# Kernel tuning notes

Measured on AMD Instinct MI355X. Metric: run time of the kernel, lower is better.

The kernel has to match this reference:

```python
import jax, jax.numpy as jnp
import numpy as np

# Vim-S config
B, L, D, DEPTH = 16, 197, 384, 24
DI, DS, DTR = 768, 16, 24  # d_inner=2*D, d_state, dt_rank=ceil(D/16)
NUM_CLASSES = 1000
EPS = 1e-5


def setup_inputs() -> dict:
    key = jax.random.key(0)
    ks = jax.random.split(key, 12)
    f = jnp.float32
    rn = lambda k, shp, s=0.02: jax.random.normal(k, shp, f) * s
    inp = {
        'x': jax.random.normal(ks[0], (B, 3, 224, 224), f),
        'patch_w': rn(ks[1], (D, 3, 16, 16)),
        'patch_b': jnp.zeros((D,), f),
        'cls_token': rn(ks[2], (1, 1, D)),
        'pos_embed': rn(ks[3], (1, L, D)),
        'in_proj_w': rn(ks[4], (DEPTH, 2 * DI, D)),
        'conv_w': rn(ks[5], (DEPTH, DI, 1, 4), 0.1),  # depthwise causal conv, d_conv=4
        'conv_b': jnp.zeros((DEPTH, DI), f),
        'x_proj_w': rn(ks[6], (DEPTH, DTR + 2 * DS, DI)),
        'dt_proj_w': rn(ks[7], (DEPTH, DI, DTR), 0.1),
        'dt_proj_b': jnp.full((DEPTH, DI), float(np.log(np.expm1(0.01))), f),
        'A_log': jnp.log(jnp.broadcast_to(jnp.arange(1, DS + 1, dtype=f), (DEPTH, DI, DS))),
        'D_ssm': jnp.ones((DEPTH, DI), f),
        'out_proj_w': rn(ks[8], (DEPTH, D, DI)),
        'norm_w': jnp.ones((DEPTH, D), f),
        'norm_b': jnp.zeros((DEPTH, D), f),
        'normf_w': jnp.ones((D,), f),
        'normf_b': jnp.zeros((D,), f),
        'head_w': rn(ks[9], (NUM_CLASSES, D)),
        'head_b': jnp.zeros((NUM_CLASSES,), f),
    }
    return inp


def _ln(u, w, b):
    mu = u.mean(-1, keepdims=True)
    v = ((u - mu) ** 2).mean(-1, keepdims=True)
    return (u - mu) * jax.lax.rsqrt(v + EPS) * w + b


def _silu(u):
    return u * jax.nn.sigmoid(u)


def _mixer(u, Win, Wc, bc, Wx, Wdt, bdt, Alog, Dp, Wout):
    # u: [B, L, D]
    xz = jnp.einsum('bld,ed->ble', u, Win)            # [B, L, 2*DI]
    xc, z = jnp.split(xz, 2, axis=-1)
    # causal depthwise conv1d (d_conv=4): pad 3 on the left
    xt = jnp.pad(xc.transpose(0, 2, 1), ((0, 0), (0, 0), (3, 0)))
    xt = jax.lax.conv_general_dilated(xt, Wc, (1,), 'VALID',
                                      dimension_numbers=('NCH', 'OIH', 'NCH'),
                                      feature_group_count=DI)
    xc = _silu((xt + bc[None, :, None]).transpose(0, 2, 1))  # [B, L, DI]
    dbl = jnp.einsum('bld,ed->ble', xc, Wx)           # [B, L, DTR+2*DS]
    dt = jax.nn.softplus(jnp.einsum('blr,dr->bld', dbl[..., :DTR], Wdt) + bdt)
    Bm = dbl[..., DTR:DTR + DS]                       # [B, L, DS]
    Cm = dbl[..., DTR + DS:]                          # [B, L, DS]
    A = -jnp.exp(Alog)                                # [DI, DS]
    dA = jnp.exp(jnp.einsum('bld,dn->bldn', dt, A))   # [B, L, DI, DS]
    dBx = jnp.einsum('bld,bln->bldn', dt * xc, Bm)    # [B, L, DI, DS]

    def step(h, inps):
        dA_t, dBx_t, C_t = inps
        h = dA_t * h + dBx_t                          # [B, DI, DS]
        return h, jnp.einsum('bdn,bn->bd', h, C_t)

    h0 = jnp.zeros((u.shape[0], DI, DS), u.dtype)
    _, ys = jax.lax.scan(step, h0, (dA.transpose(1, 0, 2, 3),
                                    dBx.transpose(1, 0, 2, 3),
                                    Cm.transpose(1, 0, 2)))
    y = ys.transpose(1, 0, 2) + xc * Dp               # [B, L, DI]
    y = y * _silu(z)
    return jnp.einsum('ble,de->bld', y, Wout)         # [B, L, D]


def reference(x, patch_w, patch_b, cls_token, pos_embed, in_proj_w, conv_w, conv_b,
              x_proj_w, dt_proj_w, dt_proj_b, A_log, D_ssm, out_proj_w,
              norm_w, norm_b, normf_w, normf_b, head_w, head_b):
    b = x.shape[0]
    # patch embed: Conv2d(3, D, 16, stride 16)
    feat = jax.lax.conv_general_dilated(x, patch_w, (16, 16), 'VALID',
                                        dimension_numbers=('NCHW', 'OIHW', 'NCHW'))
    feat = feat + patch_b[None, :, None, None]
    tokens = feat.reshape(b, D, -1).transpose(0, 2, 1)          # [B, 196, D]
    h = jnp.concatenate([jnp.broadcast_to(cls_token, (b, 1, D)), tokens], axis=1)
    h = h + pos_embed                                           # [B, 197, D]

    def layer(carry, p):
        hid, res = carry
        Win, Wc, bc, Wx, Wdt, bdt, Alog, Dp, Wout, nw, nb = p
        res = res + hid                # (hidden + residual), first layer: residual = hidden
        hid = _mixer(_ln(res, nw, nb), Win, Wc, bc, Wx, Wdt, bdt, Alog, Dp, Wout)
        return (hid, res), None

    (hid, res), _ = jax.lax.scan(layer, (h, jnp.zeros_like(h)),
                                 (in_proj_w, conv_w, conv_b, x_proj_w, dt_proj_w,
                                  dt_proj_b, A_log, D_ssm, out_proj_w, norm_w, norm_b))
    out = _ln(res + hid, normf_w, normf_b)
    return out[:, 0] @ head_w.T + head_b                        # [B, num_classes]
```

## Files before the change

kernel.cpp:

```cpp
#include <hip/hip_runtime.h>
#include <hip/hip_bf16.h>
#include <math.h>

#define BB     16
#define LL     197
#define DD     384
#define DEPTH  24
#define DI     768
#define DSN    16
#define DTR    24
#define NC     1000
#define TT     (BB*LL)
#define NPATCH 196
#define EPSV   1e-5f

#define NCHUNK 12
#define CH     17

typedef __attribute__((ext_vector_type(8))) short short8;
typedef __attribute__((ext_vector_type(4))) short short4v;
typedef __attribute__((ext_vector_type(4))) float f32x4;

__device__ __forceinline__ short f2bf(float f) {
  union { float f; unsigned u; } v; v.f = f;
  unsigned u = v.u + 0x7fffu + ((v.u >> 16) & 1u);
  return (short)(u >> 16);
}

__global__ __launch_bounds__(256) void k_cvt(const float* __restrict__ src,
                                             short* __restrict__ dst, int n) {
  int i = (blockIdx.x * 256 + threadIdx.x) * 4;
  if (i + 3 < n) {
    float4 v = *(const float4*)&src[i];
    short4v o = {f2bf(v.x), f2bf(v.y), f2bf(v.z), f2bf(v.w)};
    *(short4v*)&dst[i] = o;
  } else {
    for (int j = 0; i + j < n && j < 4; j++) dst[i + j] = f2bf(src[i + j]);
  }
}

__global__ __launch_bounds__(256) void k_init(const float* __restrict__ cls,
                                              const float* __restrict__ pos,
                                              float* __restrict__ res,
                                              float* __restrict__ hid) {
  int i = blockIdx.x * 256 + threadIdx.x;
  if (i < TT * DD) res[i] = 0.f;
  if (i < BB * DD) {
    int b = i / DD, d = i % DD;
    hid[(size_t)(b * LL) * DD + d] = cls[d] + pos[d];
  }
}

__global__ __launch_bounds__(256) void k_patch(const float* __restrict__ x,
                                               const float* __restrict__ pw,
                                               const float* __restrict__ pb,
                                               const float* __restrict__ pos,
                                               float* __restrict__ hid) {
  __shared__ short sA[64 * 40];
  __shared__ short sB[64 * 40];
  const int tid = threadIdx.x;
  const int m0 = blockIdx.x * 64, n0 = blockIdx.y * 64;
  const int srow = tid >> 2;
  const int skq = (tid & 3) * 8;
  const int lane = tid & 63, w = tid >> 6;
  const int wm = (w >> 1) * 32, wn = (w & 1) * 32;
  const int fr = lane & 15;
  const int fk = (lane >> 4) * 8;
  f32x4 acc[2][2] = {};
  const int m = m0 + srow;
  const int b = m / NPATCH;
  const int p = m % NPATCH;
  const int ph = p / 14, pwi = p % 14;
  const float* Wrow = pw + (size_t)(n0 + srow) * 768 + skq;
  for (int k0 = 0; k0 < 768; k0 += 32) {
    int k = k0 + skq;
    int c = k >> 8, rr = (k >> 4) & 15, kw = k & 15;
    const float* xrow = &x[(size_t)(((b * 3 + c) * 224) + (ph * 16 + rr)) * 224 +
                           (pwi * 16 + kw)];
    float4 a0 = *(const float4*)&xrow[0];
    float4 a1 = *(const float4*)&xrow[4];
    float4 b0 = *(const float4*)&Wrow[k0];
    float4 b1 = *(const float4*)&Wrow[k0 + 4];
    short8 av = {f2bf(a0.x), f2bf(a0.y), f2bf(a0.z), f2bf(a0.w),
                 f2bf(a1.x), f2bf(a1.y), f2bf(a1.z), f2bf(a1.w)};
    short8 bv = {f2bf(b0.x), f2bf(b0.y), f2bf(b0.z), f2bf(b0.w),
                 f2bf(b1.x), f2bf(b1.y), f2bf(b1.z), f2bf(b1.w)};
    *(short8*)&sA[srow * 40 + skq] = av;
    *(short8*)&sB[srow * 40 + skq] = bv;
    __syncthreads();
    short8 af0 = *(const short8*)&sA[(wm + fr) * 40 + fk];
    short8 af1 = *(const short8*)&sA[(wm + 16 + fr) * 40 + fk];
    short8 bf0 = *(const short8*)&sB[(wn + fr) * 40 + fk];
    short8 bf1 = *(const short8*)&sB[(wn + 16 + fr) * 40 + fk];
    acc[0][0] = __builtin_amdgcn_mfma_f32_16x16x32_bf16(af0, bf0, acc[0][0], 0, 0, 0);
    acc[0][1] = __builtin_amdgcn_mfma_f32_16x16x32_bf16(af0, bf1, acc[0][1], 0, 0, 0);
    acc[1][0] = __builtin_amdgcn_mfma_f32_16x16x32_bf16(af1, bf0, acc[1][0], 0, 0, 0);
    acc[1][1] = __builtin_amdgcn_mfma_f32_16x16x32_bf16(af1, bf1, acc[1][1], 0, 0, 0);
    __syncthreads();
  }
#pragma unroll
  for (int i = 0; i < 2; i++)
#pragma unroll
    for (int j = 0; j < 2; j++)
#pragma unroll
      for (int q = 0; q < 4; q++) {
        int mm = m0 + wm + i * 16 + (lane >> 4) * 4 + q;
        int nn = n0 + wn + j * 16 + (lane & 15);
        int b2 = mm / NPATCH, pp = mm % NPATCH;
        int tok = b2 * LL + 1 + pp;
        hid[(size_t)tok * DD + nn] = acc[i][j][q] + pb[nn] + pos[(size_t)(1 + pp) * DD + nn];
      }
}

__global__ __launch_bounds__(256) void k_gemm_bb(const short* __restrict__ A, int lda,
                                                 const short* __restrict__ W, int ldb,
                                                 float* __restrict__ C, int ldc,
                                                 int M, int N, int K) {
  __shared__ short sA[64 * 40];
  __shared__ short sB[64 * 40];
  const int tid = threadIdx.x;
  const int m0 = blockIdx.x * 64, n0 = blockIdx.y * 64;
  const int srow = tid >> 2;
  const int skq = (tid & 3) * 8;
  const int lane = tid & 63, w = tid >> 6;
  const int wm = (w >> 1) * 32, wn = (w & 1) * 32;
  const int fr = lane & 15;
  const int fk = (lane >> 4) * 8;
  f32x4 acc[2][2] = {};
  const int am = m0 + srow;
  const bool aok = am < M;
  const short* Arow = A + (size_t)am * lda + skq;
  const short* Wrow = W + (size_t)(n0 + srow) * ldb + skq;
  for (int k0 = 0; k0 < K; k0 += 32) {
    short8 av = {0, 0, 0, 0, 0, 0, 0, 0};
    if (aok) av = *(const short8*)&Arow[k0];
    short8 bv = *(const short8*)&Wrow[k0];
    *(short8*)&sA[srow * 40 + skq] = av;
    *(short8*)&sB[srow * 40 + skq] = bv;
    __syncthreads();
    short8 af0 = *(const short8*)&sA[(wm + fr) * 40 + fk];
    short8 af1 = *(const short8*)&sA[(wm + 16 + fr) * 40 + fk];
    short8 bf0 = *(const short8*)&sB[(wn + fr) * 40 + fk];
    short8 bf1 = *(const short8*)&sB[(wn + 16 + fr) * 40 + fk];
    acc[0][0] = __builtin_amdgcn_mfma_f32_16x16x32_bf16(af0, bf0, acc[0][0], 0, 0, 0);
    acc[0][1] = __builtin_amdgcn_mfma_f32_16x16x32_bf16(af0, bf1, acc[0][1], 0, 0, 0);
    acc[1][0] = __builtin_amdgcn_mfma_f32_16x16x32_bf16(af1, bf0, acc[1][0], 0, 0, 0);
    acc[1][1] = __builtin_amdgcn_mfma_f32_16x16x32_bf16(af1, bf1, acc[1][1], 0, 0, 0);
    __syncthreads();
  }
#pragma unroll
  for (int i = 0; i < 2; i++)
#pragma unroll
    for (int j = 0; j < 2; j++)
#pragma unroll
      for (int q = 0; q < 4; q++) {
        int mm = m0 + wm + i * 16 + (lane >> 4) * 4 + q;
        int nn = n0 + wn + j * 16 + (lane & 15);
        if (mm < M) C[(size_t)mm * ldc + nn] = acc[i][j][q];
      }
}

__global__ __launch_bounds__(256) void k_dtproj(const float* __restrict__ A,
                                                const short* __restrict__ W,
                                                const float* __restrict__ bias,
                                                float* __restrict__ C) {
  __shared__ short sA[64 * 40];
  __shared__ short sB[64 * 40];
  const int tid = threadIdx.x;
  const int m0 = blockIdx.x * 64, n0 = blockIdx.y * 64;
  const int srow = tid >> 2;
  const int skq = (tid & 3) * 8;
  const int lane = tid & 63, w = tid >> 6;
  const int wm = (w >> 1) * 32, wn = (w & 1) * 32;
  const int fr = lane & 15;
  const int fk = (lane >> 4) * 8;
  f32x4 acc[2][2] = {};
  const int am = m0 + srow;
  short8 av = {0, 0, 0, 0, 0, 0, 0, 0}, bv = {0, 0, 0, 0, 0, 0, 0, 0};
  if (skq < 24) {
    if (am < TT) {
      float4 a0 = *(const float4*)&A[(size_t)am * 56 + skq];
      float4 a1 = *(const float4*)&A[(size_t)am * 56 + skq + 4];
      av = short8{f2bf(a0.x), f2bf(a0.y), f2bf(a0.z), f2bf(a0.w),
                  f2bf(a1.x), f2bf(a1.y), f2bf(a1.z), f2bf(a1.w)};
    }
    bv = *(const short8*)&W[(size_t)(n0 + srow) * 24 + skq];
  }
  *(short8*)&sA[srow * 40 + skq] = av;
  *(short8*)&sB[srow * 40 + skq] = bv;
  __syncthreads();
  short8 af0 = *(const short8*)&sA[(wm + fr) * 40 + fk];
  short8 af1 = *(const short8*)&sA[(wm + 16 + fr) * 40 + fk];
  short8 bf0 = *(const short8*)&sB[(wn + fr) * 40 + fk];
  short8 bf1 = *(const short8*)&sB[(wn + 16 + fr) * 40 + fk];
  acc[0][0] = __builtin_amdgcn_mfma_f32_16x16x32_bf16(af0, bf0, acc[0][0], 0, 0, 0);
  acc[0][1] = __builtin_amdgcn_mfma_f32_16x16x32_bf16(af0, bf1, acc[0][1], 0, 0, 0);
  acc[1][0] = __builtin_amdgcn_mfma_f32_16x16x32_bf16(af1, bf0, acc[1][0], 0, 0, 0);
  acc[1][1] = __builtin_amdgcn_mfma_f32_16x16x32_bf16(af1, bf1, acc[1][1], 0, 0, 0);
#pragma unroll
  for (int i = 0; i < 2; i++)
#pragma unroll
    for (int j = 0; j < 2; j++)
#pragma unroll
      for (int q = 0; q < 4; q++) {
        int mm = m0 + wm + i * 16 + (lane >> 4) * 4 + q;
        int nn = n0 + wn + j * 16 + (lane & 15);
        if (mm < TT) {
          float v = acc[i][j][q] + bias[nn];
          v = (v > 20.f) ? v : log1pf(__expf(v));
          C[(size_t)mm * DI + nn] = v;
        }
      }
}

__global__ __launch_bounds__(256) void k_xproj(const short* __restrict__ A,
                                               const short* __restrict__ W,
                                               float* __restrict__ C) {
  __shared__ short sA[16 * 40];
  __shared__ short sB[64 * 40];
  const int tid = threadIdx.x;
  const int m0 = blockIdx.x * 16;
  const int lane = tid & 63, w = tid >> 6;
  const int wn = w * 16;
  const int fr = lane & 15;
  const int fk = (lane >> 4) * 8;
  const int srow = tid >> 2;
  const int skq = (tid & 3) * 8;
  f32x4 acc = {};
  for (int k0 = 0; k0 < DI; k0 += 32) {
    if (tid < 64) {
      *(short8*)&sA[srow * 40 + skq] =
          *(const short8*)&A[(size_t)(m0 + srow) * DI + k0 + skq];
    }
    short8 bv = {0, 0, 0, 0, 0, 0, 0, 0};
    if (srow < 56) bv = *(const short8*)&W[(size_t)srow * DI + k0 + skq];
    *(short8*)&sB[srow * 40 + skq] = bv;
    __syncthreads();
    short8 af = *(const short8*)&sA[fr * 40 + fk];
    short8 bf = *(const short8*)&sB[(wn + fr) * 40 + fk];
    acc = __builtin_amdgcn_mfma_f32_16x16x32_bf16(af, bf, acc, 0, 0, 0);
    __syncthreads();
  }
#pragma unroll
  for (int q = 0; q < 4; q++) {
    int mm = m0 + (lane >> 4) * 4 + q;
    int nn = wn + (lane & 15);
    if (nn < 56) C[(size_t)mm * 56 + nn] = acc[q];
  }
}

__global__ __launch_bounds__(128) void k_addln(float* __restrict__ res,
                                               const float* __restrict__ hid,
                                               short* __restrict__ u,
                                               const float* __restrict__ nw,
                                               const float* __restrict__ nb) {
  const int t = blockIdx.x;
  const int tid = threadIdx.x;
  float r[3];
  float s = 0.f, sq = 0.f;
#pragma unroll
  for (int j = 0; j < 3; j++) {
    int d = tid + j * 128;
    float v = res[(size_t)t * DD + d] + hid[(size_t)t * DD + d];
    res[(size_t)t * DD + d] = v;
    r[j] = v;
    s += v; sq += v * v;
  }
#pragma unroll
  for (int o = 32; o > 0; o >>= 1) { s += __shfl_xor(s, o); sq += __shfl_xor(sq, o); }
  __shared__ float ls[2], lq[2];
  int w = tid >> 6;
  if ((tid & 63) == 0) { ls[w] = s; lq[w] = sq; }
  __syncthreads();
  float st = ls[0] + ls[1], qt = lq[0] + lq[1];
  float mu = st * (1.f / 384.f);
  float var = qt * (1.f / 384.f) - mu * mu;
  float rs = rsqrtf(var + EPSV);
#pragma unroll
  for (int j = 0; j < 3; j++) {
    int d = tid + j * 128;
    u[(size_t)t * DD + d] = f2bf((r[j] - mu) * rs * nw[d] + nb[d]);
  }
}

__global__ __launch_bounds__(256) void k_conv(const float* __restrict__ xz,
                                              const float* __restrict__ wc,
                                              const float* __restrict__ bc,
                                              float* __restrict__ xc,
                                              short* __restrict__ xcbf) {
  int i = blockIdx.x * 256 + threadIdx.x;
  if (i >= TT * (DI / 4)) return;
  int eg = i % (DI / 4);
  int t = i / (DI / 4);
  int e = eg * 4;
  int b = t / LL, l = t % LL;
  const float* base = xz + (size_t)(b * LL) * (2 * DI) + e;
  float4 w0 = *(const float4*)&wc[(e + 0) * 4];
  float4 w1 = *(const float4*)&wc[(e + 1) * 4];
  float4 w2 = *(const float4*)&wc[(e + 2) * 4];
  float4 w3 = *(const float4*)&wc[(e + 3) * 4];
  float4 acc = *(const float4*)&bc[e];
  if (l >= 3) {
    float4 xv = *(const float4*)&base[(size_t)(l - 3) * (2 * DI)];
    acc.x += xv.x * w0.x; acc.y += xv.y * w1.x; acc.z += xv.z * w2.x; acc.w += xv.w * w3.x;
  }
  if (l >= 2) {
    float4 xv = *(const float4*)&base[(size_t)(l - 2) * (2 * DI)];
    acc.x += xv.x * w0.y; acc.y += xv.y * w1.y; acc.z += xv.z * w2.y; acc.w += xv.w * w3.y;
  }
  if (l >= 1) {
    float4 xv = *(const float4*)&base[(size_t)(l - 1) * (2 * DI)];
    acc.x += xv.x * w0.z; acc.y += xv.y * w1.z; acc.z += xv.z * w2.z; acc.w += xv.w * w3.z;
  }
  {
    float4 xv = *(const float4*)&base[(size_t)l * (2 * DI)];
    acc.x += xv.x * w0.w; acc.y += xv.y * w1.w; acc.z += xv.z * w2.w; acc.w += xv.w * w3.w;
  }
  acc.x = acc.x / (1.f + __expf(-acc.x));
  acc.y = acc.y / (1.f + __expf(-acc.y));
  acc.z = acc.z / (1.f + __expf(-acc.z));
  acc.w = acc.w / (1.f + __expf(-acc.w));
  *(float4*)&xc[(size_t)t * DI + e] = acc;
  short4v ov = {f2bf(acc.x), f2bf(acc.y), f2bf(acc.z), f2bf(acc.w)};
  *(short4v*)&xcbf[(size_t)t * DI + e] = ov;
}

__global__ __launch_bounds__(256) void k_scan1(const float* __restrict__ dt,
                                               const float* __restrict__ xc,
                                               const float* __restrict__ dbl,
                                               const float* __restrict__ Alog,
                                               float* __restrict__ Aprod,
                                               float* __restrict__ Hend) {
  const int tid = threadIdx.x;
  const int e = blockIdx.x * 128 + (tid >> 1);
  const int nh = tid & 1;
  const int b = blockIdx.y;
  const int c = blockIdx.z;
  float4 al0 = *(const float4*)&Alog[(size_t)e * DSN + nh * 8];
  float4 al1 = *(const float4*)&Alog[(size_t)e * DSN + nh * 8 + 4];
  float negA[8] = {-__expf(al0.x), -__expf(al0.y), -__expf(al0.z), -__expf(al0.w),
                   -__expf(al1.x), -__expf(al1.y), -__expf(al1.z), -__expf(al1.w)};
  float h[8] = {};
  float asum = 0.f;
  const int l0 = c * CH;
  const int l1 = (l0 + CH < LL) ? (l0 + CH) : LL;
  const size_t tbase = (size_t)b * LL;
  for (int l = l0; l < l1; l++) {
    size_t t = tbase + l;
    float dtv = dt[t * DI + e];
    float xcv = xc[t * DI + e];
    float4 B0 = *(const float4*)&dbl[t * 56 + DTR + nh * 8];
    float4 B1 = *(const float4*)&dbl[t * 56 + DTR + nh * 8 + 4];
    float dx = dtv * xcv;
    float Bv[8] = {B0.x, B0.y, B0.z, B0.w, B1.x, B1.y, B1.z, B1.w};
#pragma unroll
    for (int j = 0; j < 8; j++)
      h[j] = __expf(dtv * negA[j]) * h[j] + dx * Bv[j];
    asum += dtv;
  }
  size_t ci = (((size_t)c * BB + b) * DI + e) * DSN + nh * 8;
  *(float4*)&Aprod[ci] = float4{__expf(asum * negA[0]), __expf(asum * negA[1]),
                                __expf(asum * negA[2]), __expf(asum * negA[3])};
  *(float4*)&Aprod[ci + 4] = float4{__expf(asum * negA[4]), __expf(asum * negA[5]),
                                    __expf(asum * negA[6]), __expf(asum * negA[7])};
  *(float4*)&Hend[ci] = float4{h[0], h[1], h[2], h[3]};
  *(float4*)&Hend[ci + 4] = float4{h[4], h[5], h[6], h[7]};
}

__global__ __launch_bounds__(256) void k_scan2(const float* __restrict__ dt,
                                               const float* __restrict__ xc,
                                               const float* __restrict__ xz,
                                               const float* __restrict__ dbl,
                                               const float* __restrict__ Alog,
                                               const float* __restrict__ Dp,
                                               const float* __restrict__ Aprod,
                                               const float* __restrict__ Hend,
                                               short* __restrict__ ybf) {
  const int tid = threadIdx.x;
  const int e = blockIdx.x * 128 + (tid >> 1);
  const int nh = tid & 1;
  const int b = blockIdx.y;
  const int c = blockIdx.z;
  float4 al0 = *(const float4*)&Alog[(size_t)e * DSN + nh * 8];
  float4 al1 = *(const float4*)&Alog[(size_t)e * DSN + nh * 8 + 4];
  float negA[8] = {-__expf(al0.x), -__expf(al0.y), -__expf(al0.z), -__expf(al0.w),
                   -__expf(al1.x), -__expf(al1.y), -__expf(al1.z), -__expf(al1.w)};
  const float dpv = Dp[e];
  float h[8] = {};
  const size_t cstride = (size_t)BB * DI * DSN;
  const size_t cbase = (((size_t)b * DI + e) * DSN) + nh * 8;
  for (int cp = 0; cp < c; cp++) {
    size_t ci = (size_t)cp * cstride + cbase;
    float4 a0 = *(const float4*)&Aprod[ci];
    float4 a1 = *(const float4*)&Aprod[ci + 4];
    float4 e0 = *(const float4*)&Hend[ci];
    float4 e1 = *(const float4*)&Hend[ci + 4];
    h[0] = a0.x * h[0] + e0.x; h[1] = a0.y * h[1] + e0.y;
    h[2] = a0.z * h[2] + e0.z; h[3] = a0.w * h[3] + e0.w;
    h[4] = a1.x * h[4] + e1.x; h[5] = a1.y * h[5] + e1.y;
    h[6] = a1.z * h[6] + e1.z; h[7] = a1.w * h[7] + e1.w;
  }
  const int l0 = c * CH;
  const int l1 = (l0 + CH < LL) ? (l0 + CH) : LL;
  const size_t tbase = (size_t)b * LL;
  for (int l = l0; l < l1; l++) {
    size_t t = tbase + l;
    float dtv = dt[t * DI + e];
    float xcv = xc[t * DI + e];
    float zv = xz[t * (2 * DI) + DI + e];
    float4 B0 = *(const float4*)&dbl[t * 56 + DTR + nh * 8];
    float4 B1 = *(const float4*)&dbl[t * 56 + DTR + nh * 8 + 4];
    float4 C0 = *(const float4*)&dbl[t * 56 + DTR + DSN + nh * 8];
    float4 C1 = *(const float4*)&dbl[t * 56 + DTR + DSN + nh * 8 + 4];
    float dx = dtv * xcv;
    float Bv[8] = {B0.x, B0.y, B0.z, B0.w, B1.x, B1.y, B1.z, B1.w};
    float Cv[8] = {C0.x, C0.y, C0.z, C0.w, C1.x, C1.y, C1.z, C1.w};
    float acc = 0.f;
#pragma unroll
    for (int j = 0; j < 8; j++) {
      h[j] = __expf(dtv * negA[j]) * h[j] + dx * Bv[j];
      acc += h[j] * Cv[j];
    }
    acc += __shfl_xor(acc, 1);
    if (nh == 0) {
      float sz = zv * (1.f / (1.f + __expf(-zv)));
      ybf[t * DI + e] = f2bf((acc + xcv * dpv) * sz);
    }
  }
}

__global__ __launch_bounds__(256) void k_final(const float* __restrict__ res,
                                               const float* __restrict__ hid,
                                               const float* __restrict__ nfw,
                                               const float* __restrict__ nfb,
                                               const float* __restrict__ hw,
                                               const float* __restrict__ hb,
                                               float* __restrict__ out) {
  const int b = blockIdx.y;
  const int c0 = blockIdx.x * 125;
  const int tid = threadIdx.x;
  __shared__ float u0[DD];
  __shared__ float ls[4], lq[4];
  const size_t t0 = (size_t)b * LL * DD;
  float v0 = res[t0 + tid] + hid[t0 + tid];
  float v1 = (tid < 128) ? (res[t0 + 256 + tid] + hid[t0 + 256 + tid]) : 0.f;
  float s = v0 + v1, sq = v0 * v0 + v1 * v1;
#pragma unroll
  for (int o = 32; o > 0; o >>= 1) { s += __shfl_xor(s, o); sq += __shfl_xor(sq, o); }
  if ((tid & 63) == 0) { ls[tid >> 6] = s; lq[tid >> 6] = sq; }
  __syncthreads();
  float st = ls[0] + ls[1] + ls[2] + ls[3];
  float qt = lq[0] + lq[1] + lq[2] + lq[3];
  float mu = st * (1.f / 384.f);
  float var = qt * (1.f / 384.f) - mu * mu;
  float rs = rsqrtf(var + EPSV);
  u0[tid] = (v0 - mu) * rs * nfw[tid] + nfb[tid];
  if (tid < 128) u0[256 + tid] = (v1 - mu) * rs * nfw[256 + tid] + nfb[256 + tid];
  __syncthreads();
  int c = c0 + tid;
  if (tid < 125 && c < NC) {
    float acc = hb[c];
    const float* wrow = hw + (size_t)c * DD;
    for (int d = 0; d < DD; d += 4) {
      float4 w4 = *(const float4*)&wrow[d];
      acc += u0[d] * w4.x + u0[d + 1] * w4.y + u0[d + 2] * w4.z + u0[d + 3] * w4.w;
    }
    out[(size_t)b * NC + c] = acc;
  }
}

extern "C" void kernel_launch(void* const* d_in, const int* in_sizes, int n_in,
                              void* d_out, int out_size, void* d_ws, size_t ws_size,
                              hipStream_t stream) {
  const float* x       = (const float*)d_in[0];
  const float* patch_w = (const float*)d_in[1];
  const float* patch_b = (const float*)d_in[2];
  const float* cls     = (const float*)d_in[3];
  const float* pos     = (const float*)d_in[4];
  const float* in_proj = (const float*)d_in[5];
  const float* conv_w  = (const float*)d_in[6];
  const float* conv_b  = (const float*)d_in[7];
  const float* x_proj  = (const float*)d_in[8];
  const float* dt_w    = (const float*)d_in[9];
  const float* dt_b    = (const float*)d_in[10];
  const float* A_log   = (const float*)d_in[11];
  const float* D_ssm   = (const float*)d_in[12];
  const float* out_w   = (const float*)d_in[13];
  const float* norm_w  = (const float*)d_in[14];
  const float* norm_b  = (const float*)d_in[15];
  const float* normf_w = (const float*)d_in[16];
  const float* normf_b = (const float*)d_in[17];
  const float* head_w  = (const float*)d_in[18];
  const float* head_b  = (const float*)d_in[19];
  float* out = (float*)d_out;

  float* ws = (float*)d_ws;
  float* res = ws;  ws += (size_t)TT * DD;
  float* hid = ws;  ws += (size_t)TT * DD;
  float* u_r = ws;  ws += (size_t)TT * DD;
  float* xzb = ws;  ws += (size_t)TT * 2 * DI;
  float* xcb = ws;  ws += (size_t)TT * DI;
  float* dbl = ws;  ws += (size_t)TT * 56;
  float* dtb = ws;  ws += (size_t)TT * DI;
  float* crg = ws;  ws += (size_t)TT * DI;
  float* xcbf_r = ws; ws += (size_t)TT * DI / 2;
  float* ybf_r  = ws; ws += (size_t)TT * DI / 2;
  short* winbf  = (short*)ws; ws += (size_t)DEPTH * 2 * DI * DD / 2;
  short* woutbf = (short*)ws; ws += (size_t)DEPTH * DD * DI / 2;
  short* wxbf   = (short*)ws; ws += (size_t)DEPTH * 56 * DI / 2;
  short* wdtbf  = (short*)ws; ws += (size_t)DEPTH * DI * DTR / 2;

  short* u    = (short*)u_r;
  short* xcbf = (short*)xcbf_r;
  short* ybf  = (short*)ybf_r;
  float* Aprod = crg;
  float* Hend  = hid;

  {
    int n1 = DEPTH * 2 * DI * DD;
    k_cvt<<<(n1 / 4 + 255) / 256, 256, 0, stream>>>(in_proj, winbf, n1);
    int n2 = DEPTH * DD * DI;
    k_cvt<<<(n2 / 4 + 255) / 256, 256, 0, stream>>>(out_w, woutbf, n2);
    int n3 = DEPTH * 56 * DI;
    k_cvt<<<(n3 / 4 + 255) / 256, 256, 0, stream>>>(x_proj, wxbf, n3);
    int n4 = DEPTH * DI * DTR;
    k_cvt<<<(n4 / 4 + 255) / 256, 256, 0, stream>>>(dt_w, wdtbf, n4);
  }

  k_init<<<(TT * DD + 255) / 256, 256, 0, stream>>>(cls, pos, res, hid);
  k_patch<<<dim3(49, 6), 256, 0, stream>>>(x, patch_w, patch_b, pos, hid);

  for (int layer = 0; layer < DEPTH; layer++) {
    k_addln<<<TT, 128, 0, stream>>>(res, hid, u, norm_w + layer * DD, norm_b + layer * DD);
    k_gemm_bb<<<dim3(50, 24), 256, 0, stream>>>(
        u, DD, winbf + (size_t)layer * 2 * DI * DD, DD, xzb, 2 * DI, TT, 2 * DI, DD);
    k_conv<<<(TT * (DI / 4) + 255) / 256, 256, 0, stream>>>(
        xzb, conv_w + layer * DI * 4, conv_b + layer * DI, xcb, xcbf);
    k_xproj<<<dim3(TT / 16), 256, 0, stream>>>(
        xcbf, wxbf + (size_t)layer * 56 * DI, dbl);
    k_dtproj<<<dim3(50, 12), 256, 0, stream>>>(
        dbl, wdtbf + (size_t)layer * DI * DTR, dt_b + layer * DI, dtb);
    k_scan1<<<dim3(DI / 128, BB, NCHUNK), 256, 0, stream>>>(
        dtb, xcb, dbl, A_log + (size_t)layer * DI * DSN, Aprod, Hend);
    k_scan2<<<dim3(DI / 128, BB, NCHUNK), 256, 0, stream>>>(
        dtb, xcb, xzb, dbl, A_log + (size_t)layer * DI * DSN,
        D_ssm + layer * DI, Aprod, Hend, ybf);
    k_gemm_bb<<<dim3(50, 6), 256, 0, stream>>>(
        ybf, DI, woutbf + (size_t)layer * DD * DI, DI, hid, DD, TT, DD, DI);
  }

  k_final<<<dim3(8, BB), 256, 0, stream>>>(res, hid, normf_w, normf_b, head_w, head_b, out);
}
```

Before: 2.864 ms.

## Use direct global-to-LDS loads and 128x128 tiles for in_proj GEMM

Replaces the register-staged GEMM with kernels that load A and W tiles straight into LDS via global_load_lds. The in_proj GEMM moves to a 128x128 tile with a 4x4 MFMA accumulator per wave, which raises reuse per LDS load. The out_proj GEMM keeps 64x64 tiles but uses the direct LDS load. The first scan pass also skips its last chunk, presumably because that chunk's carry is never consumed. Padded LDS rows are dropped, which may add bank conflicts. The row bounds guard on A loads is removed, so reads past M=3152 depend on the buffer being large enough.

```diff
diff --git a/kernel.cpp b/kernel.cpp
--- a/kernel.cpp
+++ b/kernel.cpp
@@ -25,6 +25,12 @@
   union { float f; unsigned u; } v; v.f = f;
   unsigned u = v.u + 0x7fffu + ((v.u >> 16) & 1u);
   return (short)(u >> 16);
+}
+
+__device__ __forceinline__ void gload16(const short* g, const short* l) {
+  __builtin_amdgcn_global_load_lds(
+      (const __attribute__((address_space(1))) unsigned int*)g,
+      (__attribute__((address_space(3))) unsigned int*)l, 16, 0, 0);
 }
 
 __global__ __launch_bounds__(256) void k_cvt(const float* __restrict__ src,
@@ -112,36 +118,83 @@
       }
 }
 
-__global__ __launch_bounds__(256) void k_gemm_bb(const short* __restrict__ A, int lda,
+__global__ __launch_bounds__(256) void k_gemm128(const short* __restrict__ A, int lda,
                                                  const short* __restrict__ W, int ldb,
                                                  float* __restrict__ C, int ldc,
                                                  int M, int N, int K) {
-  __shared__ short sA[64 * 40];
-  __shared__ short sB[64 * 40];
-  const int tid = threadIdx.x;
+  __shared__ short sA[128 * 32];
+  __shared__ short sB[128 * 32];
+  const int tid = threadIdx.x;
+  const int lane = tid & 63, w = tid >> 6;
+  const int m0 = blockIdx.x * 128, n0 = blockIdx.y * 128;
+  const int wm = (w >> 1) * 64, wn = (w & 1) * 64;
+  const int fr = lane & 15;
+  const int fk = (lane >> 4) * 8;
+  const int q0 = w * 2, q1 = w * 2 + 1;
+  const int sr0 = q0 * 16 + (lane >> 2);
+  const int sr1 = q1 * 16 + (lane >> 2);
+  const int scol = (lane & 3) * 8;
+  f32x4 acc[4][4] = {};
+  const short* Ab0 = A + (size_t)(m0 + sr0) * lda + scol;
+  const short* Ab1 = A + (size_t)(m0 + sr1) * lda + scol;
+  const short* Bb0 = W + (size_t)(n0 + sr0) * ldb + scol;
+  const short* Bb1 = W + (size_t)(n0 + sr1) * ldb + scol;
+  for (int k0 = 0; k0 < K; k0 += 32) {
+    gload16(Ab0 + k0, &sA[q0 * 512]);
+    gload16(Ab1 + k0, &sA[q1 * 512]);
+    gload16(Bb0 + k0, &sB[q0 * 512]);
+    gload16(Bb1 + k0, &sB[q1 * 512]);
+    __syncthreads();
+    short8 af[4], bf[4];
+#pragma unroll
+    for (int i = 0; i < 4; i++) {
+      af[i] = *(const short8*)&sA[(wm + i * 16 + fr) * 32 + fk];
+      bf[i] = *(const short8*)&sB[(wn + i * 16 + fr) * 32 + fk];
+    }
+#pragma unroll
+    for (int i = 0; i < 4; i++)
+#pragma unroll
+      for (int j = 0; j < 4; j++)
+        acc[i][j] = __builtin_amdgcn_mfma_f32_16x16x32_bf16(af[i], bf[j], acc[i][j], 0, 0, 0);
+    __syncthreads();
+  }
+#pragma unroll
+  for (int i = 0; i < 4; i++)
+#pragma unroll
+    for (int j = 0; j < 4; j++)
+#pragma unroll
+      for (int q = 0; q < 4; q++) {
+        int mm = m0 + wm + i * 16 + (lane >> 4) * 4 + q;
+        int nn = n0 + wn + j * 16 + fr;
+        if (mm < M) C[(size_t)mm * ldc + nn] = acc[i][j][q];
+      }
+}
+
+__global__ __launch_bounds__(256) void k_gemm64(const short* __restrict__ A, int lda,
+                                                const short* __restrict__ W, int ldb,
+                                                float* __restrict__ C, int ldc,
+                                                int M, int N, int K) {
+  __shared__ short sA[64 * 32];
+  __shared__ short sB[64 * 32];
+  const int tid = threadIdx.x;
+  const int lane = tid & 63, w = tid >> 6;
   const int m0 = blockIdx.x * 64, n0 = blockIdx.y * 64;
-  const int srow = tid >> 2;
-  const int skq = (tid & 3) * 8;
-  const int lane = tid & 63, w = tid >> 6;
   const int wm = (w >> 1) * 32, wn = (w & 1) * 32;
   const int fr = lane & 15;
   const int fk = (lane >> 4) * 8;
+  const int srow = w * 16 + (lane >> 2);
+  const int scol = (lane & 3) * 8;
   f32x4 acc[2][2] = {};
-  const int am = m0 + srow;
-  const bool aok = am < M;
-  const short* Arow = A + (size_t)am * lda + skq;
-  const short* Wrow = W + (size_t)(n0 + srow) * ldb + skq;
+  const short* Ab = A + (size_t)(m0 + srow) * lda + scol;
+  const short* Bb = W + (size_t)(n0 + srow) * ldb + scol;
   for (int k0 = 0; k0 < K; k0 += 32) {
-    short8 av = {0, 0, 0, 0, 0, 0, 0, 0};
-    if (aok) av = *(const short8*)&Arow[k0];
-    short8 bv = *(const short8*)&Wrow[k0];
-    *(short8*)&sA[srow * 40 + skq] = av;
-    *(short8*)&sB[srow * 40 + skq] = bv;
-    __syncthreads();
-    short8 af0 = *(const short8*)&sA[(wm + fr) * 40 + fk];
-    short8 af1 = *(const short8*)&sA[(wm + 16 + fr) * 40 + fk];
-    short8 bf0 = *(const short8*)&sB[(wn + fr) * 40 + fk];
-    short8 bf1 = *(const short8*)&sB[(wn + 16 + fr) * 40 + fk];
+    gload16(Ab + k0, &sA[w * 512]);
+    gload16(Bb + k0, &sB[w * 512]);
+    __syncthreads();
+    short8 af0 = *(const short8*)&sA[(wm + fr) * 32 + fk];
+    short8 af1 = *(const short8*)&sA[(wm + 16 + fr) * 32 + fk];
+    short8 bf0 = *(const short8*)&sB[(wn + fr) * 32 + fk];
+    short8 bf1 = *(const short8*)&sB[(wn + 16 + fr) * 32 + fk];
     acc[0][0] = __builtin_amdgcn_mfma_f32_16x16x32_bf16(af0, bf0, acc[0][0], 0, 0, 0);
     acc[0][1] = __builtin_amdgcn_mfma_f32_16x16x32_bf16(af0, bf1, acc[0][1], 0, 0, 0);
     acc[1][0] = __builtin_amdgcn_mfma_f32_16x16x32_bf16(af1, bf0, acc[1][0], 0, 0, 0);
@@ -155,7 +208,7 @@
 #pragma unroll
       for (int q = 0; q < 4; q++) {
         int mm = m0 + wm + i * 16 + (lane >> 4) * 4 + q;
-        int nn = n0 + wn + j * 16 + (lane & 15);
+        int nn = n0 + wn + j * 16 + fr;
         if (mm < M) C[(size_t)mm * ldc + nn] = acc[i][j][q];
       }
 }
@@ -532,7 +585,7 @@
 
   for (int layer = 0; layer < DEPTH; layer++) {
     k_addln<<<TT, 128, 0, stream>>>(res, hid, u, norm_w + layer * DD, norm_b + layer * DD);
-    k_gemm_bb<<<dim3(50, 24), 256, 0, stream>>>(
+    k_gemm128<<<dim3(25, 12), 256, 0, stream>>>(
         u, DD, winbf + (size_t)layer * 2 * DI * DD, DD, xzb, 2 * DI, TT, 2 * DI, DD);
     k_conv<<<(TT * (DI / 4) + 255) / 256, 256, 0, stream>>>(
         xzb, conv_w + layer * DI * 4, conv_b + layer * DI, xcb, xcbf);
@@ -540,12 +593,12 @@
         xcbf, wxbf + (size_t)layer * 56 * DI, dbl);
     k_dtproj<<<dim3(50, 12), 256, 0, stream>>>(
         dbl, wdtbf + (size_t)layer * DI * DTR, dt_b + layer * DI, dtb);
-    k_scan1<<<dim3(DI / 128, BB, NCHUNK), 256, 0, stream>>>(
+    k_scan1<<<dim3(DI / 128, BB, NCHUNK - 1), 256, 0, stream>>>(
         dtb, xcb, dbl, A_log + (size_t)layer * DI * DSN, Aprod, Hend);
     k_scan2<<<dim3(DI / 128, BB, NCHUNK), 256, 0, stream>>>(
         dtb, xcb, xzb, dbl, A_log + (size_t)layer * DI * DSN,
         D_ssm + layer * DI, Aprod, Hend, ybf);
-    k_gemm_bb<<<dim3(50, 6), 256, 0, stream>>>(
+    k_gemm64<<<dim3(50, 6), 256, 0, stream>>>(
         ybf, DI, woutbf + (size_t)layer * DD * DI, DI, hid, DD, TT, DD, DI);
   }
 
```

New measurement: 2.918 ms. No clear change (+1.9%).
